# Kernel tuning notes

Hardware: AMD Instinct MI355X
Metric: run time of the kernel (lower is better)

The kernel has to match this reference:

```python
import jax, jax.numpy as jnp
import numpy as np

N, M, D_IN, D_OUT = 8192, 8192, 512, 512


def setup_inputs() -> dict:
    key = jax.random.key(0)
    k1, k2, k3, k4 = jax.random.split(key, 4)
    return {
        "x": jax.random.normal(k1, (N, D_OUT), dtype=jnp.float32),
        "mu": jax.random.normal(k2, (M, D_IN), dtype=jnp.float32),
        "W": jax.random.normal(k3, (D_OUT, D_IN), dtype=jnp.float32),
        "b": jax.random.normal(k4, (D_OUT,), dtype=jnp.float32),
    }


def reference(x, mu, W, b):
    # f_mu: (M, D_out) -- projection + nonlinearity (func = tanh)
    f_mu = jnp.tanh(mu @ W.T + b)
    # measure m[n, m] = -0.5 * ||x_n - f_mu_m||^2, via the matmul expansion
    # (avoids the (N, M, D) diff tensor; same math as sum of squared diffs)
    x_sq = jnp.sum(x * x, axis=-1)            # (N,)
    f_sq = jnp.sum(f_mu * f_mu, axis=-1)      # (M,)
    cross = x @ f_mu.T                        # (N, M)
    m = -0.5 * (x_sq[:, None] - 2.0 * cross + f_sq[None, :])
    # energy: -sum over rows of logsumexp over axis 1
    return -jnp.sum(jax.nn.logsumexp(m, axis=1))
```

## Files before the change

### kernel.cpp

```cpp
#include <hip/hip_runtime.h>

#define D 512
#define NROWS 8192
#define MROWS 8192
#define NCHUNK 8
#define CHUNK_COLS (MROWS / NCHUNK)
#define SWEEPS (CHUNK_COLS / 256)
#define NRB (NROWS / 128)
#define LOG2E 1.4426950408889634f
#define LN2 0.6931471805599453f

typedef float floatx4 __attribute__((ext_vector_type(4)));
typedef __bf16 bf16x8 __attribute__((ext_vector_type(8)));
typedef unsigned uintx4 __attribute__((ext_vector_type(4)));
typedef int intx8 __attribute__((ext_vector_type(8)));

typedef __attribute__((address_space(1))) void* as1_void_p;
typedef __attribute__((address_space(3))) void* as3_void_p;

__device__ __forceinline__ void async_cp16(const void* g, void* l) {
    __builtin_amdgcn_global_load_lds((as1_void_p)(void*)g, (as3_void_p)l, 16, 0, 0);
}

__device__ __forceinline__ unsigned short f2bf(float f) {
    unsigned u = __float_as_uint(f);
    u += 0x7fffu + ((u >> 16) & 1u);
    return (unsigned short)(u >> 16);
}
__device__ __forceinline__ float bf2f(unsigned short h) {
    return __uint_as_float(((unsigned)h) << 16);
}

__device__ __forceinline__ float fast_tanh(float x) {
    const float xc = fminf(fmaxf(x, -15.0f), 15.0f);
    const float e = __builtin_exp2f(xc * (2.0f * LOG2E));
    return (e - 1.0f) * __builtin_amdgcn_rcpf(e + 1.0f);
}

__device__ __forceinline__ unsigned pack2(float a, float b) {
    return (unsigned)f2bf(a) | ((unsigned)f2bf(b) << 16);
}

#define MUBLK (MROWS * D / 2048)
#define WBLK (D * D / 2048)
__global__ void k_convmw(const float* __restrict__ mu,
                         const float* __restrict__ W,
                         unsigned short* __restrict__ mub,
                         unsigned short* __restrict__ Wb,
                         float* __restrict__ fsq,
                         float* __restrict__ out) {
    const int bid = blockIdx.x;
    const int t = threadIdx.x;
    if (bid < MUBLK) {
        const size_t i = ((size_t)bid * 256 + t) * 2;
        const float4 v0 = ((const float4*)mu)[i];
        const float4 v1 = ((const float4*)mu)[i + 1];
        uintx4 o;
        o.x = pack2(v0.x, v0.y); o.y = pack2(v0.z, v0.w);
        o.z = pack2(v1.x, v1.y); o.w = pack2(v1.z, v1.w);
        ((uintx4*)mub)[i / 2] = o;
    } else {
        const int wb = bid - MUBLK;
        if (wb == 0 && t == 0) out[0] = 0.f;
        const size_t i = ((size_t)wb * 256 + t) * 2;
        const float4 v0 = ((const float4*)W)[i];
        const float4 v1 = ((const float4*)W)[i + 1];
        uintx4 o;
        o.x = pack2(v0.x, v0.y); o.y = pack2(v0.z, v0.w);
        o.z = pack2(v1.x, v1.y); o.w = pack2(v1.z, v1.w);
        ((uintx4*)Wb)[i / 2] = o;
        if (t < 64) fsq[wb * 64 + t] = 0.f;
    }
}

#define FGB 512
#define XBLK (NROWS / 4)
__global__ __launch_bounds__(256, 2)
void k_fgemm_xprep(const unsigned short* __restrict__ mub,
                   const unsigned short* __restrict__ Wb,
                   const float* __restrict__ bias,
                   const float* __restrict__ x,
                   unsigned char* __restrict__ fb8,
                   unsigned char* __restrict__ xb8,
                   float* __restrict__ fsq,
                   float* __restrict__ xsq) {
    const int bid = blockIdx.x;
    const int tid = threadIdx.x;

    if (bid >= FGB) {
        const int row = (bid - FGB) * 4 + (tid >> 6);
        const int lane = tid & 63;
        const float4 v0 = ((const float4*)(x + (size_t)row * D))[lane * 2];
        const float4 v1 = ((const float4*)(x + (size_t)row * D))[lane * 2 + 1];
        int p0 = 0, p1 = 0;
        p0 = __builtin_amdgcn_cvt_pk_fp8_f32(v0.x * LOG2E, v0.y * LOG2E, p0, false);
        p0 = __builtin_amdgcn_cvt_pk_fp8_f32(v0.z * LOG2E, v0.w * LOG2E, p0, true);
        p1 = __builtin_amdgcn_cvt_pk_fp8_f32(v1.x * LOG2E, v1.y * LOG2E, p1, false);
        p1 = __builtin_amdgcn_cvt_pk_fp8_f32(v1.z * LOG2E, v1.w * LOG2E, p1, true);
        uint2 o; o.x = (unsigned)p0; o.y = (unsigned)p1;
        ((uint2*)(xb8 + (size_t)row * D))[lane] = o;
        float q, s = 0.f;
        q = __builtin_amdgcn_cvt_f32_fp8(p0, 0); s += q * q;
        q = __builtin_amdgcn_cvt_f32_fp8(p0, 1); s += q * q;
        q = __builtin_amdgcn_cvt_f32_fp8(p0, 2); s += q * q;
        q = __builtin_amdgcn_cvt_f32_fp8(p0, 3); s += q * q;
        q = __builtin_amdgcn_cvt_f32_fp8(p1, 0); s += q * q;
        q = __builtin_amdgcn_cvt_f32_fp8(p1, 1); s += q * q;
        q = __builtin_amdgcn_cvt_f32_fp8(p1, 2); s += q * q;
        q = __builtin_amdgcn_cvt_f32_fp8(p1, 3); s += q * q;
        #pragma unroll
        for (int m = 1; m < 64; m <<= 1) s += __shfl_xor(s, m);
        if (lane == 0) xsq[row] = s;
        return;
    }

    __shared__ unsigned short Ab[128 * 32];
    __shared__ unsigned short Bb[64 * 32];

    const int wave = tid >> 6;
    const int lane = tid & 63;
    const int wr = wave >> 1, wc = wave & 1;
    const int g = lane >> 4;
    const int lm = lane & 15;

    const int row0 = (bid & 63) * 128;
    const int col0 = (bid >> 6) * 64;

    const int srow = tid >> 2;
    const int gsrc = (tid & 3) ^ ((srow >> 1) & 3);
    const unsigned short* gA = mub + (size_t)(row0 + srow) * D + gsrc * 8;
    const unsigned short* gB = Wb  + (size_t)(col0 + srow) * D + gsrc * 8;
    char* lA = ((char*)Ab) + wave * 1024;
    char* lB = ((char*)Bb) + wave * 1024;

    const int xsel = (lm >> 1) & 3;
    const unsigned short* fragA = Ab + (64 * wr + lm) * 32 + (g ^ xsel) * 8;
    const unsigned short* fragB = Bb + (32 * wc + lm) * 32 + (g ^ xsel) * 8;

    floatx4 acc[4][2];
    const floatx4 zz = {0.f, 0.f, 0.f, 0.f};
    #pragma unroll
    for (int i = 0; i < 4; ++i)
        #pragma unroll
        for (int j = 0; j < 2; ++j) acc[i][j] = zz;

    for (int kt = 0; kt < 16; ++kt) {
        const int k0 = kt * 32;
        async_cp16(gA + k0, lA);
        async_cp16(gA + 64 * D + k0, lA + 4096);
        async_cp16(gB + k0, lB);
        __syncthreads();
        bf16x8 af[4], bfr[2];
        #pragma unroll
        for (int i = 0; i < 4; ++i) af[i] = *(const bf16x8*)(fragA + i * 512);
        #pragma unroll
        for (int j = 0; j < 2; ++j) bfr[j] = *(const bf16x8*)(fragB + j * 512);
        #pragma unroll
        for (int i = 0; i < 4; ++i)
            #pragma unroll
            for (int j = 0; j < 2; ++j)
                acc[i][j] = __builtin_amdgcn_mfma_f32_16x16x32_bf16(af[i], bfr[j], acc[i][j], 0, 0, 0);
        __syncthreads();
    }

    float bcol[2];
    #pragma unroll
    for (int j = 0; j < 2; ++j) bcol[j] = bias[col0 + 32 * wc + 16 * j + lm];
    #pragma unroll
    for (int i = 0; i < 4; ++i) {
        #pragma unroll
        for (int r = 0; r < 4; ++r) {
            const int row = row0 + 64 * wr + 16 * i + 4 * g + r;
            float sq = 0.f;
            #pragma unroll
            for (int j = 0; j < 2; ++j) {
                const int col = col0 + 32 * wc + 16 * j + lm;
                const float tv = fast_tanh(acc[i][j][r] + bcol[j]);
                const int pk = __builtin_amdgcn_cvt_pk_fp8_f32(tv, tv, 0, false);
                fb8[(size_t)row * D + col] = (unsigned char)(pk & 0xff);
                const float qf = __builtin_amdgcn_cvt_f32_fp8(pk, 0);
                sq += qf * qf;
            }
            #pragma unroll
            for (int d = 1; d < 16; d <<= 1) sq += __shfl_xor(sq, d);
            if (lm == 0) atomicAdd(fsq + row, sq);
        }
    }
}

__global__ __launch_bounds__(256, 2)
void k_cross(const unsigned char* __restrict__ xb8,
             const unsigned char* __restrict__ fb8,
             const float* __restrict__ fsq,
             float* __restrict__ pmax,
             float* __restrict__ psum) {
    __shared__ char Ab[128 * 128];
    __shared__ char Bb[256 * 128];
    __shared__ float mbuf[128], sbuf[128];

    const int tid = threadIdx.x;
    const int wave = tid >> 6;
    const int lane = tid & 63;
    const int wr = wave >> 1, wc = wave & 1;
    const int g = lane >> 4;
    const int lm = lane & 15;

    const int row0 = blockIdx.x * 128;
    const int chunk = blockIdx.y;

    const unsigned char* pA[4];
    char* dA[4];
    size_t offB[8];
    char* dB[8];
    #pragma unroll
    for (int p = 0; p < 4; ++p) {
        const int row = 32 * wave + 8 * p + (lane >> 3);
        const int srcg = (lane & 7) ^ ((row >> 1) & 7);
        pA[p] = xb8 + (size_t)(row0 + row) * D + srcg * 16;
        dA[p] = Ab + wave * 4096 + p * 1024 + lane * 16;
    }
    #pragma unroll
    for (int p = 0; p < 8; ++p) {
        const int row = 64 * wave + 8 * p + (lane >> 3);
        const int srcg = (lane & 7) ^ ((row >> 1) & 7);
        offB[p] = (size_t)row * D + srcg * 16;
        dB[p] = Bb + wave * 8192 + p * 1024 + lane * 16;
    }

    const int f8 = (lm >> 1) & 7;
    const int pg0 = ((2 * g) ^ f8) * 16;
    const char* fragA = Ab + (64 * wr + lm) * 128;
    const char* fragB = Bb + (128 * wc + lm) * 128;

    float m_loc[4][4], s_loc[4][4];
    #pragma unroll
    for (int i = 0; i < 4; ++i)
        #pragma unroll
        for (int r = 0; r < 4; ++r) { m_loc[i][r] = -__builtin_inff(); s_loc[i][r] = 0.f; }

    for (int st = 0; st < SWEEPS; ++st) {
        const int col0 = chunk * CHUNK_COLS + st * 256;
        const unsigned char* gBbase = fb8 + (size_t)col0 * D;

        floatx4 acc[4][8];
        const floatx4 zz = {0.f, 0.f, 0.f, 0.f};
        #pragma unroll
        for (int i = 0; i < 4; ++i)
            #pragma unroll
            for (int j = 0; j < 8; ++j) acc[i][j] = zz;

        for (int kt = 0; kt < 4; ++kt) {
            const int k0 = kt * 128;
            #pragma unroll
            for (int p = 0; p < 4; ++p) async_cp16(pA[p] + k0, dA[p]);
            #pragma unroll
            for (int p = 0; p < 8; ++p) async_cp16(gBbase + offB[p] + k0, dB[p]);
            __syncthreads();

            intx8 av[4];
            #pragma unroll
            for (int i = 0; i < 4; ++i) {
                const char* pa = fragA + i * 2048;
                const int4 lo = *(const int4*)(pa + pg0);
                const int4 hi = *(const int4*)(pa + (pg0 ^ 16));
                av[i] = (intx8){lo.x, lo.y, lo.z, lo.w, hi.x, hi.y, hi.z, hi.w};
            }
            #pragma unroll
            for (int j = 0; j < 8; ++j) {
                const char* pb = fragB + j * 2048;
                const int4 lo = *(const int4*)(pb + pg0);
                const int4 hi = *(const int4*)(pb + (pg0 ^ 16));
                const intx8 bv = {lo.x, lo.y, lo.z, lo.w, hi.x, hi.y, hi.z, hi.w};
                acc[0][j] = __builtin_amdgcn_mfma_scale_f32_16x16x128_f8f6f4(
                    av[0], bv, acc[0][j], 0, 0, 0, 0x7f7f7f7f, 0, 0x7f7f7f7f);
                acc[1][j] = __builtin_amdgcn_mfma_scale_f32_16x16x128_f8f6f4(
                    av[1], bv, acc[1][j], 0, 0, 0, 0x7f7f7f7f, 0, 0x7f7f7f7f);
                acc[2][j] = __builtin_amdgcn_mfma_scale_f32_16x16x128_f8f6f4(
                    av[2], bv, acc[2][j], 0, 0, 0, 0x7f7f7f7f, 0, 0x7f7f7f7f);
                acc[3][j] = __builtin_amdgcn_mfma_scale_f32_16x16x128_f8f6f4(
                    av[3], bv, acc[3][j], 0, 0, 0, 0x7f7f7f7f, 0, 0x7f7f7f7f);
            }
            __syncthreads();
        }

        float hf[8];
        #pragma unroll
        for (int j = 0; j < 8; ++j)
            hf[j] = 0.5f * LOG2E * fsq[col0 + 128 * wc + 16 * j + lm];
        #pragma unroll
        for (int i = 0; i < 4; ++i) {
            #pragma unroll
            for (int r = 0; r < 4; ++r) {
                float v[8];
                float mm = -__builtin_inff();
                #pragma unroll
                for (int j = 0; j < 8; ++j) {
                    v[j] = acc[i][j][r] - hf[j];
                    mm = fmaxf(mm, v[j]);
                }
                const float nm = fmaxf(m_loc[i][r], mm);
                float s = s_loc[i][r] * __builtin_exp2f(m_loc[i][r] - nm);
                #pragma unroll
                for (int j = 0; j < 8; ++j) s += __builtin_exp2f(v[j] - nm);
                s_loc[i][r] = s;
                m_loc[i][r] = nm;
            }
        }
    }

    #pragma unroll
    for (int i = 0; i < 4; ++i) {
        #pragma unroll
        for (int r = 0; r < 4; ++r) {
            float m = m_loc[i][r], s = s_loc[i][r];
            #pragma unroll
            for (int d = 1; d < 16; d <<= 1) {
                const float om = __shfl_xor(m, d);
                const float os = __shfl_xor(s, d);
                const float nm = fmaxf(m, om);
                s = s * __builtin_exp2f(m - nm) + os * __builtin_exp2f(om - nm);
                m = nm;
            }
            m_loc[i][r] = m; s_loc[i][r] = s;
        }
    }
    if (wc == 0 && lm == 0) {
        #pragma unroll
        for (int i = 0; i < 4; ++i)
            #pragma unroll
            for (int r = 0; r < 4; ++r) {
                const int rl = 64 * wr + 16 * i + 4 * g + r;
                mbuf[rl] = m_loc[i][r]; sbuf[rl] = s_loc[i][r];
            }
    }
    __syncthreads();
    if (wc == 1 && lm == 0) {
        #pragma unroll
        for (int i = 0; i < 4; ++i)
            #pragma unroll
            for (int r = 0; r < 4; ++r) {
                const int rl = 64 * wr + 16 * i + 4 * g + r;
                const float om = mbuf[rl], os = sbuf[rl];
                float m = m_loc[i][r], s = s_loc[i][r];
                const float nm = fmaxf(m, om);
                s = s * __builtin_exp2f(m - nm) + os * __builtin_exp2f(om - nm);
                pmax[(size_t)(row0 + rl) * NCHUNK + chunk] = nm;
                psum[(size_t)(row0 + rl) * NCHUNK + chunk] = s;
            }
    }
}

__global__ void k_finish(const float* __restrict__ pmax,
                         const float* __restrict__ psum,
                         const float* __restrict__ xsq,
                         float* __restrict__ out) {
    const int row = blockIdx.x * 256 + threadIdx.x;
    const float4* pm4 = (const float4*)(pmax + (size_t)row * NCHUNK);
    const float4* ps4 = (const float4*)(psum + (size_t)row * NCHUNK);
    float pm[NCHUNK], ps[NCHUNK];
    #pragma unroll
    for (int c = 0; c < NCHUNK / 4; ++c) {
        const float4 a = pm4[c], b = ps4[c];
        pm[4*c] = a.x; pm[4*c+1] = a.y; pm[4*c+2] = a.z; pm[4*c+3] = a.w;
        ps[4*c] = b.x; ps[4*c+1] = b.y; ps[4*c+2] = b.z; ps[4*c+3] = b.w;
    }
    float gm = -__builtin_inff();
    #pragma unroll
    for (int c = 0; c < NCHUNK; ++c) gm = fmaxf(gm, pm[c]);
    float s = 0.f;
    #pragma unroll
    for (int c = 0; c < NCHUNK; ++c) s += ps[c] * __builtin_exp2f(pm[c] - gm);
    float lse = LN2 * (gm + __builtin_log2f(s)) - 0.5f * (LN2 * LN2) * xsq[row];
    #pragma unroll
    for (int m = 1; m < 64; m <<= 1) lse += __shfl_xor(lse, m);
    __shared__ float ws4[4];
    if ((threadIdx.x & 63) == 0) ws4[threadIdx.x >> 6] = lse;
    __syncthreads();
    if (threadIdx.x == 0) atomicAdd(out, -(ws4[0] + ws4[1] + ws4[2] + ws4[3]));
}

extern "C" void kernel_launch(void* const* d_in, const int* in_sizes, int n_in,
                              void* d_out, int out_size, void* d_ws, size_t ws_size,
                              hipStream_t stream) {
    const float* x  = (const float*)d_in[0];
    const float* mu = (const float*)d_in[1];
    const float* W  = (const float*)d_in[2];
    const float* b  = (const float*)d_in[3];

    char* ws = (char*)d_ws;
    unsigned char*  xb8 = (unsigned char*)(ws);
    unsigned char*  fb8 = (unsigned char*)(ws + (4u << 20));
    unsigned short* mub = (unsigned short*)(ws + (8u << 20));
    unsigned short* Wb  = (unsigned short*)(ws + (16u << 20));
    float* xsq  = (float*)(ws + (17u << 20));
    float* fsq  = xsq + NROWS;
    float* pmax = fsq + MROWS;
    float* psum = pmax + (size_t)NROWS * NCHUNK;

    float* out = (float*)d_out;

    hipLaunchKernelGGL(k_convmw, dim3(MUBLK + WBLK), dim3(256), 0, stream,
                       mu, W, mub, Wb, fsq, out);
    hipLaunchKernelGGL(k_fgemm_xprep, dim3(FGB + XBLK), dim3(256), 0, stream,
                       mub, Wb, b, x, fb8, xb8, fsq, xsq);
    hipLaunchKernelGGL(k_cross, dim3(NRB, NCHUNK), dim3(256), 0, stream,
                       xb8, fb8, fsq, pmax, psum);
    hipLaunchKernelGGL(k_finish, dim3(NROWS / 256), dim3(256), 0, stream,
                       pmax, psum, xsq, out);
}
```

Baseline: 150.6 us.

## Fuse fp32-to-bf16 conversion of mu and W into the projection GEMM

Removes the separate conversion kernel that wrote bf16 copies of mu and W. The projection GEMM now streams fp32 tiles straight into LDS with async loads and converts them to bf16 fragments in registers before the MFMA. Zeroing of fsq and the output moves to memset calls. The LDS swizzle in the cross kernel is also simplified to a per-lane XOR. This saves one launch and the bf16 round trip through global memory, but doubles the LDS footprint and read traffic in the GEMM and adds conversion ALU work in its inner loop.

```diff
diff --git a/kernel.cpp b/kernel.cpp
--- a/kernel.cpp
+++ b/kernel.cpp
@@ -27,9 +27,6 @@
     u += 0x7fffu + ((u >> 16) & 1u);
     return (unsigned short)(u >> 16);
 }
-__device__ __forceinline__ float bf2f(unsigned short h) {
-    return __uint_as_float(((unsigned)h) << 16);
-}
 
 __device__ __forceinline__ float fast_tanh(float x) {
     const float xc = fminf(fmaxf(x, -15.0f), 15.0f);
@@ -41,43 +38,18 @@
     return (unsigned)f2bf(a) | ((unsigned)f2bf(b) << 16);
 }
 
-#define MUBLK (MROWS * D / 2048)
-#define WBLK (D * D / 2048)
-__global__ void k_convmw(const float* __restrict__ mu,
-                         const float* __restrict__ W,
-                         unsigned short* __restrict__ mub,
-                         unsigned short* __restrict__ Wb,
-                         float* __restrict__ fsq,
-                         float* __restrict__ out) {
-    const int bid = blockIdx.x;
-    const int t = threadIdx.x;
-    if (bid < MUBLK) {
-        const size_t i = ((size_t)bid * 256 + t) * 2;
-        const float4 v0 = ((const float4*)mu)[i];
-        const float4 v1 = ((const float4*)mu)[i + 1];
-        uintx4 o;
-        o.x = pack2(v0.x, v0.y); o.y = pack2(v0.z, v0.w);
-        o.z = pack2(v1.x, v1.y); o.w = pack2(v1.z, v1.w);
-        ((uintx4*)mub)[i / 2] = o;
-    } else {
-        const int wb = bid - MUBLK;
-        if (wb == 0 && t == 0) out[0] = 0.f;
-        const size_t i = ((size_t)wb * 256 + t) * 2;
-        const float4 v0 = ((const float4*)W)[i];
-        const float4 v1 = ((const float4*)W)[i + 1];
-        uintx4 o;
-        o.x = pack2(v0.x, v0.y); o.y = pack2(v0.z, v0.w);
-        o.z = pack2(v1.x, v1.y); o.w = pack2(v1.z, v1.w);
-        ((uintx4*)Wb)[i / 2] = o;
-        if (t < 64) fsq[wb * 64 + t] = 0.f;
-    }
+__device__ __forceinline__ bf16x8 cvt8(const float4 lo, const float4 hi) {
+    uintx4 u;
+    u.x = pack2(lo.x, lo.y); u.y = pack2(lo.z, lo.w);
+    u.z = pack2(hi.x, hi.y); u.w = pack2(hi.z, hi.w);
+    return *(bf16x8*)&u;
 }
 
 #define FGB 512
 #define XBLK (NROWS / 4)
 __global__ __launch_bounds__(256, 2)
-void k_fgemm_xprep(const unsigned short* __restrict__ mub,
-                   const unsigned short* __restrict__ Wb,
+void k_fgemm_xprep(const float* __restrict__ mu,
+                   const float* __restrict__ W,
                    const float* __restrict__ bias,
                    const float* __restrict__ x,
                    unsigned char* __restrict__ fb8,
@@ -114,8 +86,8 @@
         return;
     }
 
-    __shared__ unsigned short Ab[128 * 32];
-    __shared__ unsigned short Bb[64 * 32];
+    __shared__ char Afp[128 * 128];
+    __shared__ char Bfp[64 * 128];
 
     const int wave = tid >> 6;
     const int lane = tid & 63;
@@ -126,16 +98,28 @@
     const int row0 = (bid & 63) * 128;
     const int col0 = (bid >> 6) * 64;
 
-    const int srow = tid >> 2;
-    const int gsrc = (tid & 3) ^ ((srow >> 1) & 3);
-    const unsigned short* gA = mub + (size_t)(row0 + srow) * D + gsrc * 8;
-    const unsigned short* gB = Wb  + (size_t)(col0 + srow) * D + gsrc * 8;
-    char* lA = ((char*)Ab) + wave * 1024;
-    char* lB = ((char*)Bb) + wave * 1024;
-
-    const int xsel = (lm >> 1) & 3;
-    const unsigned short* fragA = Ab + (64 * wr + lm) * 32 + (g ^ xsel) * 8;
-    const unsigned short* fragB = Bb + (32 * wc + lm) * 32 + (g ^ xsel) * 8;
+    const int srcg = (lane & 7) ^ (lane >> 3);
+    const char* pA[4];
+    char* dA[4];
+    #pragma unroll
+    for (int p = 0; p < 4; ++p) {
+        const int row = 32 * wave + 8 * p + (lane >> 3);
+        pA[p] = (const char*)(mu + (size_t)(row0 + row) * D) + srcg * 16;
+        dA[p] = Afp + wave * 4096 + p * 1024 + lane * 16;
+    }
+    const char* pB[2];
+    char* dB[2];
+    #pragma unroll
+    for (int p = 0; p < 2; ++p) {
+        const int row = 16 * wave + 8 * p + (lane >> 3);
+        pB[p] = (const char*)(W + (size_t)(col0 + row) * D) + srcg * 16;
+        dB[p] = Bfp + wave * 2048 + p * 1024 + lane * 16;
+    }
+
+    const int f8 = lm & 7;
+    const int q0 = ((2 * g) ^ f8) * 16;
+    const char* fragA = Afp + (64 * wr + lm) * 128;
+    const char* fragB = Bfp + (32 * wc + lm) * 128;
 
     floatx4 acc[4][2];
     const floatx4 zz = {0.f, 0.f, 0.f, 0.f};
@@ -145,16 +129,23 @@
         for (int j = 0; j < 2; ++j) acc[i][j] = zz;
 
     for (int kt = 0; kt < 16; ++kt) {
-        const int k0 = kt * 32;
-        async_cp16(gA + k0, lA);
-        async_cp16(gA + 64 * D + k0, lA + 4096);
-        async_cp16(gB + k0, lB);
+        const int k0 = kt * 128;
+        #pragma unroll
+        for (int p = 0; p < 4; ++p) async_cp16(pA[p] + k0, dA[p]);
+        #pragma unroll
+        for (int p = 0; p < 2; ++p) async_cp16(pB[p] + k0, dB[p]);
         __syncthreads();
         bf16x8 af[4], bfr[2];
         #pragma unroll
-        for (int i = 0; i < 4; ++i) af[i] = *(const bf16x8*)(fragA + i * 512);
-        #pragma unroll
-        for (int j = 0; j < 2; ++j) bfr[j] = *(const bf16x8*)(fragB + j * 512);
+        for (int i = 0; i < 4; ++i) {
+            const char* pa = fragA + i * 2048;
+            af[i] = cvt8(*(const float4*)(pa + q0), *(const float4*)(pa + (q0 ^ 16)));
+        }
+        #pragma unroll
+        for (int j = 0; j < 2; ++j) {
+            const char* pb = fragB + j * 2048;
+            bfr[j] = cvt8(*(const float4*)(pb + q0), *(const float4*)(pb + (q0 ^ 16)));
+        }
         #pragma unroll
         for (int i = 0; i < 4; ++i)
             #pragma unroll
@@ -208,6 +199,7 @@
     const int row0 = blockIdx.x * 128;
     const int chunk = blockIdx.y;
 
+    const int srcg = (lane & 7) ^ (lane >> 3);
     const unsigned char* pA[4];
     char* dA[4];
     size_t offB[8];
@@ -215,19 +207,17 @@
     #pragma unroll
     for (int p = 0; p < 4; ++p) {
         const int row = 32 * wave + 8 * p + (lane >> 3);
-        const int srcg = (lane & 7) ^ ((row >> 1) & 7);
         pA[p] = xb8 + (size_t)(row0 + row) * D + srcg * 16;
         dA[p] = Ab + wave * 4096 + p * 1024 + lane * 16;
     }
     #pragma unroll
     for (int p = 0; p < 8; ++p) {
         const int row = 64 * wave + 8 * p + (lane >> 3);
-        const int srcg = (lane & 7) ^ ((row >> 1) & 7);
         offB[p] = (size_t)row * D + srcg * 16;
         dB[p] = Bb + wave * 8192 + p * 1024 + lane * 16;
     }
 
-    const int f8 = (lm >> 1) & 7;
+    const int f8 = lm & 7;
     const int pg0 = ((2 * g) ^ f8) * 16;
     const char* fragA = Ab + (64 * wr + lm) * 128;
     const char* fragB = Bb + (128 * wc + lm) * 128;
@@ -388,21 +378,19 @@
     const float* b  = (const float*)d_in[3];
 
     char* ws = (char*)d_ws;
-    unsigned char*  xb8 = (unsigned char*)(ws);
-    unsigned char*  fb8 = (unsigned char*)(ws + (4u << 20));
-    unsigned short* mub = (unsigned short*)(ws + (8u << 20));
-    unsigned short* Wb  = (unsigned short*)(ws + (16u << 20));
-    float* xsq  = (float*)(ws + (17u << 20));
+    unsigned char* xb8 = (unsigned char*)(ws);
+    unsigned char* fb8 = (unsigned char*)(ws + (4u << 20));
+    float* xsq  = (float*)(ws + (8u << 20));
     float* fsq  = xsq + NROWS;
     float* pmax = fsq + MROWS;
     float* psum = pmax + (size_t)NROWS * NCHUNK;
 
     float* out = (float*)d_out;
 
-    hipLaunchKernelGGL(k_convmw, dim3(MUBLK + WBLK), dim3(256), 0, stream,
-                       mu, W, mub, Wb, fsq, out);
+    hipMemsetAsync(fsq, 0, MROWS * sizeof(float), stream);
+    hipMemsetAsync(out, 0, sizeof(float), stream);
     hipLaunchKernelGGL(k_fgemm_xprep, dim3(FGB + XBLK), dim3(256), 0, stream,
-                       mub, Wb, b, x, fb8, xb8, fsq, xsq);
+                       mu, W, b, x, fb8, xb8, fsq, xsq);
     hipLaunchKernelGGL(k_cross, dim3(NRB, NCHUNK), dim3(256), 0, stream,
                        xb8, fb8, fsq, pmax, psum);
     hipLaunchKernelGGL(k_finish, dim3(NROWS / 256), dim3(256), 0, stream,
```

Measured after the change: 158.2 us. 1.05x slower.

## Halve K-loop barriers in projection GEMM and change LDS swizzle in energy kernel

Applied to the files above, without the earlier changes.

The projection GEMM now loads two 32-wide K slices into two LDS buffers per iteration, cutting the loop from 16 to 8 steps and halving the number of __syncthreads barriers. The energy kernel's LDS XOR swizzle is changed from using (row>>1)&7 to row&7, so source groups are permuted per row to reduce bank conflicts on fragment reads. The trade is more LDS per block in the GEMM, and a swizzle whose read side must match the write side exactly.

```diff
diff --git a/kernel.cpp b/kernel.cpp
--- a/kernel.cpp
+++ b/kernel.cpp
@@ -26,9 +26,6 @@
     unsigned u = __float_as_uint(f);
     u += 0x7fffu + ((u >> 16) & 1u);
     return (unsigned short)(u >> 16);
-}
-__device__ __forceinline__ float bf2f(unsigned short h) {
-    return __uint_as_float(((unsigned)h) << 16);
 }
 
 __device__ __forceinline__ float fast_tanh(float x) {
@@ -114,8 +111,8 @@
         return;
     }
 
-    __shared__ unsigned short Ab[128 * 32];
-    __shared__ unsigned short Bb[64 * 32];
+    __shared__ unsigned short Ab[2][128 * 32];
+    __shared__ unsigned short Bb[2][64 * 32];
 
     const int wave = tid >> 6;
     const int lane = tid & 63;
@@ -130,12 +127,14 @@
     const int gsrc = (tid & 3) ^ ((srow >> 1) & 3);
     const unsigned short* gA = mub + (size_t)(row0 + srow) * D + gsrc * 8;
     const unsigned short* gB = Wb  + (size_t)(col0 + srow) * D + gsrc * 8;
-    char* lA = ((char*)Ab) + wave * 1024;
-    char* lB = ((char*)Bb) + wave * 1024;
+    char* lA0 = ((char*)Ab[0]) + wave * 1024;
+    char* lA1 = ((char*)Ab[1]) + wave * 1024;
+    char* lB0 = ((char*)Bb[0]) + wave * 1024;
+    char* lB1 = ((char*)Bb[1]) + wave * 1024;
 
     const int xsel = (lm >> 1) & 3;
-    const unsigned short* fragA = Ab + (64 * wr + lm) * 32 + (g ^ xsel) * 8;
-    const unsigned short* fragB = Bb + (32 * wc + lm) * 32 + (g ^ xsel) * 8;
+    const unsigned short* fragA0 = Ab[0] + (64 * wr + lm) * 32 + (g ^ xsel) * 8;
+    const unsigned short* fragB0 = Bb[0] + (32 * wc + lm) * 32 + (g ^ xsel) * 8;
 
     floatx4 acc[4][2];
     const floatx4 zz = {0.f, 0.f, 0.f, 0.f};
@@ -144,22 +143,30 @@
         #pragma unroll
         for (int j = 0; j < 2; ++j) acc[i][j] = zz;
 
-    for (int kt = 0; kt < 16; ++kt) {
-        const int k0 = kt * 32;
-        async_cp16(gA + k0, lA);
-        async_cp16(gA + 64 * D + k0, lA + 4096);
-        async_cp16(gB + k0, lB);
+    for (int kt = 0; kt < 8; ++kt) {
+        const int k0 = kt * 64;
+        async_cp16(gA + k0, lA0);
+        async_cp16(gA + 64 * D + k0, lA0 + 4096);
+        async_cp16(gB + k0, lB0);
+        async_cp16(gA + k0 + 32, lA1);
+        async_cp16(gA + 64 * D + k0 + 32, lA1 + 4096);
+        async_cp16(gB + k0 + 32, lB1);
         __syncthreads();
-        bf16x8 af[4], bfr[2];
-        #pragma unroll
-        for (int i = 0; i < 4; ++i) af[i] = *(const bf16x8*)(fragA + i * 512);
-        #pragma unroll
-        for (int j = 0; j < 2; ++j) bfr[j] = *(const bf16x8*)(fragB + j * 512);
-        #pragma unroll
-        for (int i = 0; i < 4; ++i)
-            #pragma unroll
-            for (int j = 0; j < 2; ++j)
-                acc[i][j] = __builtin_amdgcn_mfma_f32_16x16x32_bf16(af[i], bfr[j], acc[i][j], 0, 0, 0);
+        #pragma unroll
+        for (int h = 0; h < 2; ++h) {
+            const unsigned short* fA = fragA0 + h * 4096;
+            const unsigned short* fB = fragB0 + h * 2048;
+            bf16x8 af[4], bfr[2];
+            #pragma unroll
+            for (int i = 0; i < 4; ++i) af[i] = *(const bf16x8*)(fA + i * 512);
+            #pragma unroll
+            for (int j = 0; j < 2; ++j) bfr[j] = *(const bf16x8*)(fB + j * 512);
+            #pragma unroll
+            for (int i = 0; i < 4; ++i)
+                #pragma unroll
+                for (int j = 0; j < 2; ++j)
+                    acc[i][j] = __builtin_amdgcn_mfma_f32_16x16x32_bf16(af[i], bfr[j], acc[i][j], 0, 0, 0);
+        }
         __syncthreads();
     }
 
@@ -208,6 +215,7 @@
     const int row0 = blockIdx.x * 128;
     const int chunk = blockIdx.y;
 
+    const int srcg = (lane & 7) ^ (lane >> 3);
     const unsigned char* pA[4];
     char* dA[4];
     size_t offB[8];
@@ -215,19 +223,17 @@
     #pragma unroll
     for (int p = 0; p < 4; ++p) {
         const int row = 32 * wave + 8 * p + (lane >> 3);
-        const int srcg = (lane & 7) ^ ((row >> 1) & 7);
         pA[p] = xb8 + (size_t)(row0 + row) * D + srcg * 16;
         dA[p] = Ab + wave * 4096 + p * 1024 + lane * 16;
     }
     #pragma unroll
     for (int p = 0; p < 8; ++p) {
         const int row = 64 * wave + 8 * p + (lane >> 3);
-        const int srcg = (lane & 7) ^ ((row >> 1) & 7);
         offB[p] = (size_t)row * D + srcg * 16;
         dB[p] = Bb + wave * 8192 + p * 1024 + lane * 16;
     }
 
-    const int f8 = (lm >> 1) & 7;
+    const int f8 = lm & 7;
     const int pg0 = ((2 * g) ^ f8) * 16;
     const char* fragA = Ab + (64 * wr + lm) * 128;
     const char* fragB = Bb + (128 * wc + lm) * 128;
```

Measured after the change: 146.8 us. 1.03x faster.
